# Kernel tuning notes

Measured on AMD Instinct MI355X. Metric: run time of the kernel, lower is better.

## Reference

```python
import jax, jax.numpy as jnp
import numpy as np

B, S, D = 4, 4096, 256


def setup_inputs() -> dict:
    key = jax.random.key(0)
    k1, k2, k3 = jax.random.split(key, 3)
    x = jax.random.normal(k1, (B, S, D), dtype=jnp.float32)
    w_int = jax.random.randint(k2, (D, D), 0, 127, dtype=jnp.int32)  # quantized weight (out, in)
    scale = jax.random.uniform(k3, (D,), dtype=jnp.float32)          # per-output-channel scale
    return {"x": x, "w_int": w_int, "scale": scale}


def reference(x, w_int, scale):
    # self-attention: q = k = v = x, single head over feature dim D
    inv_sqrt_d = 1.0 / jnp.sqrt(jnp.asarray(D, dtype=x.dtype))
    scores = jnp.einsum('bqd,bkd->bqk', x, x) * inv_sqrt_d   # [B,S,S]
    probs = jax.nn.softmax(scores, axis=-1)
    attn = jnp.einsum('bqk,bkd->bqd', probs, x)              # [B,S,D]
    # quantized linear: dequantize then matmul (y = attn @ W^T)
    W = w_int.astype(x.dtype) * scale[:, None]               # [D_out, D_in]
    return jnp.einsum('bsd,od->bso', attn, W)
```

## Files before the change

### kernel.cpp

```cpp
#include <hip/hip_runtime.h>

typedef __bf16 bf16x8 __attribute__((ext_vector_type(8)));
typedef float f32x16 __attribute__((ext_vector_type(16)));
typedef unsigned short u16x8 __attribute__((ext_vector_type(8)));

constexpr int B = 4, S = 4096, D = 256;
constexpr float CSC = 0.09016844005556021f;

static __device__ __forceinline__ unsigned short f2bf(float f) {
  unsigned int u = __builtin_bit_cast(unsigned int, f);
  u = (u + 0x7fffu + ((u >> 16) & 1u)) >> 16;
  return (unsigned short)u;
}

static __device__ __forceinline__ float bf2f(unsigned short u) {
  unsigned int v = ((unsigned int)u) << 16;
  return __builtin_bit_cast(float, v);
}

static __device__ __forceinline__ unsigned int pk2bf(float lo, float hi) {
  unsigned int r;
  asm("v_cvt_pk_bf16_f32 %0, %1, %2" : "=v"(r) : "v"(lo), "v"(hi));
  return r;
}

static __device__ __forceinline__ void gld16(const void* g, void* l) {
  __builtin_amdgcn_global_load_lds(
      (const __attribute__((address_space(1))) unsigned int*)g,
      (__attribute__((address_space(3))) unsigned int*)l, 16, 0, 0);
}

#define FENCE_V4()                                                \
  do {                                                            \
    asm volatile("s_waitcnt vmcnt(4) lgkmcnt(0)" ::: "memory");   \
    __builtin_amdgcn_s_barrier();                                 \
    asm volatile("" ::: "memory");                                \
  } while (0)
#define FENCE_V8()                                                \
  do {                                                            \
    asm volatile("s_waitcnt vmcnt(8) lgkmcnt(0)" ::: "memory");   \
    __builtin_amdgcn_s_barrier();                                 \
    asm volatile("" ::: "memory");                                \
  } while (0)
#define FENCE_LG()                                                \
  do {                                                            \
    asm volatile("s_waitcnt lgkmcnt(0)" ::: "memory");            \
    __builtin_amdgcn_s_barrier();                                 \
    asm volatile("" ::: "memory");                                \
  } while (0)
#define FENCE_ALL0()                                              \
  do {                                                            \
    asm volatile("s_waitcnt vmcnt(0) lgkmcnt(0)" ::: "memory");   \
    __builtin_amdgcn_s_barrier();                                 \
    asm volatile("" ::: "memory");                                \
  } while (0)

__global__ __launch_bounds__(256) void k_prep(const float* __restrict__ x,
                                              unsigned short* __restrict__ xK,
                                              unsigned short* __restrict__ xV) {
  __shared__ unsigned short T[64][72];
  __shared__ unsigned short R[64][72];
  int bid = blockIdx.x;
  int b = bid >> 8, rem = bid & 255;
  int s0 = (rem >> 2) * 64, d0 = (rem & 3) * 64;
  int j = threadIdx.x & 63, i0 = threadIdx.x >> 6;
#pragma unroll
  for (int k = 0; k < 16; ++k) {
    int i = k * 4 + i0;
    int idx = (b * S + s0 + i) * D + d0 + j;
    unsigned short v = f2bf(x[idx]);
    T[j][i] = v;
    R[i][j] = v;
  }
  __syncthreads();
  int t = s0 >> 6;
#pragma unroll
  for (int p = 0; p < 2; ++p) {
    int cc = p * 256 + threadIdx.x;
    int sl8 = cc >> 6, row = cc & 63;
    u16x8 v = *(const u16x8*)&R[row][sl8 * 8];
    int dg = d0 + sl8 * 8;
    int s = dg >> 4, hi = (dg >> 3) & 1;
    size_t off = ((((size_t)(b * 64 + t) * 16 + s) * 2 + hi) * 64 + row) * 8;
    *(u16x8*)(xK + off) = v;
  }
#pragma unroll
  for (int p = 0; p < 2; ++p) {
    int cc = p * 256 + threadIdx.x;
    int c = cc >> 7, hi = (cc >> 6) & 1, dl = cc & 63;
    u16x8 v = *(const u16x8*)&T[dl][c * 16 + hi * 8];
    size_t off = ((((size_t)(b * 64 + t) * 4 + c) * 2 + hi) * 256 + (d0 + dl)) * 8;
    *(u16x8*)(xV + off) = v;
  }
}

__global__ __launch_bounds__(256) void k_deqw(const int* __restrict__ w,
                                              unsigned short* __restrict__ wK) {
  int o = blockIdx.x, d = threadIdx.x;
  unsigned short v = f2bf((float)w[o * 256 + d]);
  wK[(((d >> 4) * 2 + ((d >> 3) & 1)) * 256 + o) * 8 + (d & 7)] = v;
}

__global__ __launch_bounds__(512, 2) void k_attn(const unsigned short* __restrict__ xK,
                                                 const unsigned short* __restrict__ xV,
                                                 unsigned short* __restrict__ PO0,
                                                 unsigned short* __restrict__ PO1,
                                                 float* __restrict__ ML) {
  __shared__ __align__(16) char smem[132096];

  int tid = threadIdx.x;
  int w = tid >> 6, lane = tid & 63;
  int q5 = lane & 31, hi = lane >> 5;
  int pair = w >> 1, dh = w & 1;

  int bid = blockIdx.x;
  int swz = (bid & 7) * 32 + (bid >> 3);
  int h = swz & 1;
  int qg = swz >> 1;
  int q0 = qg * 128;
  int bat = q0 >> 12;
  int qloc = q0 & (S - 1);

  int qrow = qloc + pair * 32 + q5;
  const unsigned short* Qb =
      xK + (size_t)(bat * 64 + (qrow >> 6)) * 16384 + hi * 512 + (qrow & 63) * 8;
  bf16x8 qf[16];
#pragma unroll
  for (int s = 0; s < 16; ++s) qf[s] = *(const bf16x8*)(Qb + s * 1024);

  f32x16 acc[8];
#pragma unroll
  for (int dt = 0; dt < 8; ++dt)
#pragma unroll
    for (int j = 0; j < 16; ++j) acc[dt][j] = 0.f;
  float l_lane = 0.f;
  unsigned int paw[8];

  const char* xKb = (const char*)xK + (size_t)(bat * 64 + h * 32) * 32768;
  const char* xVb = (const char*)xV + (size_t)(bat * 64 + h * 32) * 32768;

  auto STAGE_K = [&](int itile, int bb) {
    char* Kd = smem + bb * 32768;
    const char* srcK = xKb + (size_t)itile * 32768;
#pragma unroll
    for (int i = 0; i < 4; ++i) {
      int off = (w * 2 + (i >> 1)) * 2048 + (i & 1) * 1024;
      gld16(srcK + off + lane * 16, Kd + off);
    }
  };
  auto STAGE_V = [&](int itile, int bb) {
    char* Vd = smem + 65536 + bb * 32768;
    const char* srcV = xVb + (size_t)itile * 32768;
#pragma unroll
    for (int i = 0; i < 4; ++i) {
      int off = (w >> 1) * 8192 + ((w & 1) * 4 + i) * 1024;
      gld16(srcV + off + lane * 16, Vd + off);
    }
  };

  auto QK = [&](int bb, f32x16& st) {
    const char* Kt = smem + bb * 32768 + hi * 1024 + dh * 512 + q5 * 16;
#pragma unroll
    for (int j = 0; j < 16; ++j) st[j] = 0.f;
    __builtin_amdgcn_s_setprio(1);
#pragma unroll
    for (int s = 0; s < 16; ++s) {
      bf16x8 kf = *(const bf16x8*)(Kt + s * 2048);
      st = __builtin_amdgcn_mfma_f32_32x32x16_bf16(kf, qf[s], st, 0, 0, 0);
    }
    __builtin_amdgcn_s_setprio(0);
  };
  auto PV = [&](int bb) {
    union PA { unsigned int u[4]; bf16x8 v; };
    PA pa0, pa1;
    pa0.u[0] = paw[0]; pa0.u[1] = paw[1]; pa0.u[2] = paw[2]; pa0.u[3] = paw[3];
    pa1.u[0] = paw[4]; pa1.u[1] = paw[5]; pa1.u[2] = paw[6]; pa1.u[3] = paw[7];
    __builtin_amdgcn_s_setprio(1);
#pragma unroll
    for (int s2i = 0; s2i < 2; ++s2i) {
      const char* Vt = smem + 65536 + bb * 32768 + (dh * 2 + s2i) * 8192 +
                       hi * 4096 + q5 * 16;
      bf16x8 pa = (s2i == 0) ? pa0.v : pa1.v;
#pragma unroll
      for (int dt = 0; dt < 8; ++dt) {
        bf16x8 vf = *(const bf16x8*)(Vt + dt * 512);
        acc[dt] = __builtin_amdgcn_mfma_f32_32x32x16_bf16(vf, pa, acc[dt], 0, 0, 0);
      }
    }
    __builtin_amdgcn_s_setprio(0);
  };
  auto SM = [&](const f32x16& st) {
    unsigned int pk[8];
    float ps = 0.f;
#pragma unroll
    for (int a = 0; a < 8; ++a) {
      float lo = exp2f(st[2 * a] * CSC);
      float hh = exp2f(st[2 * a + 1] * CSC);
      ps += lo + hh;
      pk[a] = pk2bf(lo, hh);
    }
    l_lane += ps;
    unsigned int a0 = pk[0], b0 = pk[2];
    unsigned int a1 = pk[1], b1 = pk[3];
    unsigned int a2 = pk[4], b2 = pk[6];
    unsigned int a3 = pk[5], b3 = pk[7];
    asm volatile("v_permlane32_swap_b32 %0, %1" : "+v"(a0), "+v"(b0));
    asm volatile("v_permlane32_swap_b32 %0, %1" : "+v"(a1), "+v"(b1));
    asm volatile("v_permlane32_swap_b32 %0, %1" : "+v"(a2), "+v"(b2));
    asm volatile("v_permlane32_swap_b32 %0, %1" : "+v"(a3), "+v"(b3));
    paw[0] = a0; paw[1] = a1; paw[2] = b0; paw[3] = b1;
    paw[4] = a2; paw[5] = a3; paw[6] = b2; paw[7] = b3;
  };

  STAGE_K(0, 0);
  STAGE_V(0, 0);
  STAGE_K(1, 1);
  FENCE_V8();
  {
    f32x16 st;
    QK(0, st);
    SM(st);
  }
  STAGE_V(1, 1);

  for (int t = 1; t < 32; ++t) {
    int cur = t & 1;
    FENCE_V4();
    if (t < 31) STAGE_K(t + 1, cur ^ 1);
    f32x16 st;
    QK(cur, st);
    PV(cur ^ 1);
    SM(st);
    FENCE_LG();
    if (t < 31) STAGE_V(t + 1, cur ^ 1);
  }

  FENCE_ALL0();
  PV(1);

  float lw = l_lane + __shfl_xor(l_lane, 32, 64);
  float* LX = (float*)(smem + 131072);
  if (lane < 32) LX[w * 32 + q5] = lw;
  __syncthreads();
  float l_tot = lw + LX[(w ^ 1) * 32 + q5];
  if (dh == 0 && lane < 32) {
    int row = q0 + pair * 32 + q5;
    ML[((size_t)h * 16384 + row) * 2 + 0] = 0.f;
    ML[((size_t)h * 16384 + row) * 2 + 1] = l_tot;
  }
  __syncthreads();

  unsigned short* Pb2 = (h == 0) ? PO0 : PO1;
#pragma unroll
  for (int rh = 0; rh < 2; ++rh) {
    float* slot = (float*)(smem + w * 16384);
#pragma unroll
    for (int dt4 = 0; dt4 < 4; ++dt4) {
#pragma unroll
      for (int r = 0; r < 16; ++r) {
        int dloc = dt4 * 32 + (r & 3) + 8 * (r >> 2) + 4 * hi;
        slot[dloc * 32 + q5] = acc[rh * 4 + dt4][r];
      }
    }
    __syncthreads();
    if (dh == rh) {
      const float* pslot = (const float*)(smem + (w ^ 1) * 16384);
#pragma unroll
      for (int dt4 = 0; dt4 < 4; ++dt4) {
#pragma unroll
        for (int r = 0; r < 16; ++r) {
          int dloc = dt4 * 32 + (r & 3) + 8 * (r >> 2) + 4 * hi;
          acc[rh * 4 + dt4][r] += pslot[dloc * 32 + q5];
        }
      }
      char* E = smem + w * 16384;
#pragma unroll
      for (int dt4 = 0; dt4 < 4; ++dt4) {
#pragma unroll
        for (int a = 0; a < 4; ++a) {
          int dl = dt4 * 32 + 8 * a + 4 * hi;
          *(unsigned int*)(E + q5 * 272 + dl * 2) =
              pk2bf(acc[rh * 4 + dt4][4 * a + 0], acc[rh * 4 + dt4][4 * a + 1]);
          *(unsigned int*)(E + q5 * 272 + dl * 2 + 4) =
              pk2bf(acc[rh * 4 + dt4][4 * a + 2], acc[rh * 4 + dt4][4 * a + 3]);
        }
      }
      asm volatile("s_waitcnt lgkmcnt(0)" ::: "memory");
#pragma unroll
      for (int i = 0; i < 8; ++i) {
        int qr = i * 4 + (lane >> 4);
        int ch = lane & 15;
        u16x8 v = *(const u16x8*)(E + qr * 272 + ch * 16);
        *(u16x8*)(Pb2 + (size_t)(q0 + pair * 32 + qr) * 256 + rh * 128 + ch * 8) = v;
      }
    }
    __syncthreads();
  }
}

__global__ __launch_bounds__(512, 2) void k_gemm(const unsigned short* __restrict__ PO0,
                                                 const unsigned short* __restrict__ PO1,
                                                 const float* __restrict__ ML,
                                                 const unsigned short* __restrict__ wK,
                                                 const float* __restrict__ scale,
                                                 float* __restrict__ out) {
  __shared__ __align__(16) char Wl[131072];
  int tid = threadIdx.x;
  int w = tid >> 6, lane = tid & 63;
  int q5 = lane & 31, hi = lane >> 5;
  int msub = w & 1, oq = w >> 1;
  int m0 = blockIdx.x * 64;

#pragma unroll
  for (int i = 0; i < 16; ++i) {
    int off = (i * 512 + tid) * 16;
    gld16((const char*)wK + off, Wl + off);
  }

  int row = m0 + msub * 32 + q5;
  float il = 1.f / (ML[(size_t)row * 2 + 1] + ML[((size_t)16384 + row) * 2 + 1]);

  bf16x8 af[16];
#pragma unroll
  for (int s = 0; s < 16; ++s) {
    u16x8 a0 = *(const u16x8*)(PO0 + (size_t)row * 256 + s * 16 + hi * 8);
    u16x8 a1 = *(const u16x8*)(PO1 + (size_t)row * 256 + s * 16 + hi * 8);
    union { unsigned int u[4]; bf16x8 v; } cv;
#pragma unroll
    for (int e = 0; e < 4; ++e) {
      float lo = (bf2f(a0[2 * e]) + bf2f(a1[2 * e])) * il;
      float hh = (bf2f(a0[2 * e + 1]) + bf2f(a1[2 * e + 1])) * il;
      cv.u[e] = pk2bf(lo, hh);
    }
    af[s] = cv.v;
  }

  asm volatile("s_waitcnt vmcnt(0)" ::: "memory");
  __builtin_amdgcn_s_barrier();

  f32x16 acc[2];
#pragma unroll
  for (int t = 0; t < 2; ++t)
#pragma unroll
    for (int j = 0; j < 16; ++j) acc[t][j] = 0.f;

#pragma unroll
  for (int t = 0; t < 2; ++t) {
    int obase = (oq * 2 + t) * 32;
    const char* Wt = Wl + hi * 4096 + (obase + q5) * 16;
#pragma unroll
    for (int s = 0; s < 16; ++s) {
      bf16x8 wf = *(const bf16x8*)(Wt + s * 8192);
      acc[t] = __builtin_amdgcn_mfma_f32_32x32x16_bf16(af[s], wf, acc[t], 0, 0, 0);
    }
  }

#pragma unroll
  for (int t = 0; t < 2; ++t) {
    int o = (oq * 2 + t) * 32 + q5;
    float sc = scale[o];
#pragma unroll
    for (int r = 0; r < 16; ++r) {
      int mr = m0 + msub * 32 + (r & 3) + 8 * (r >> 2) + 4 * hi;
      out[(size_t)mr * 256 + o] = acc[t][r] * sc;
    }
  }
}

extern "C" void kernel_launch(void* const* d_in, const int* in_sizes, int n_in,
                              void* d_out, int out_size, void* d_ws, size_t ws_size,
                              hipStream_t stream) {
  (void)in_sizes; (void)n_in; (void)out_size; (void)ws_size;
  const float* x = (const float*)d_in[0];
  const int* w_int = (const int*)d_in[1];
  const float* scale = (const float*)d_in[2];
  float* out = (float*)d_out;

  char* ws = (char*)d_ws;
  unsigned short* xK  = (unsigned short*)(ws);
  unsigned short* xV  = (unsigned short*)(ws + 8388608);
  unsigned short* wK  = (unsigned short*)(ws + 16777216);
  float*          ML  = (float*)(ws + 16908288);
  unsigned short* PO0 = (unsigned short*)(ws + 17170432);
  unsigned short* PO1 = (unsigned short*)(ws + 25559040);

  k_prep<<<dim3(1024), dim3(256), 0, stream>>>(x, xK, xV);
  k_deqw<<<dim3(256), dim3(256), 0, stream>>>(w_int, wK);
  k_attn<<<dim3(256), dim3(512), 0, stream>>>(xK, xV, PO0, PO1, ML);
  k_gemm<<<dim3(256), dim3(512), 0, stream>>>(PO0, PO1, ML, wK, scale, out);
}
```

Before: 101.3 us.

## Triple-buffer V tiles to drop the mid-iteration barrier in attention loop

The V shared-memory staging moves from double to triple buffering, which grows LDS to 160 KB. K and V for the next tile are now issued together at the top of each iteration. This removes the second lgkmcnt wait plus workgroup barrier that previously sat between PV/softmax and staging the next V tile. The cost is extra LDS, which rules out co-residency of a second block. The vmcnt-based fence logic still covers correctness because the pending loads are always the just-issued tile.

```diff
diff --git a/kernel.cpp b/kernel.cpp
--- a/kernel.cpp
+++ b/kernel.cpp
@@ -42,12 +42,6 @@
     __builtin_amdgcn_s_barrier();                                 \
     asm volatile("" ::: "memory");                                \
   } while (0)
-#define FENCE_LG()                                                \
-  do {                                                            \
-    asm volatile("s_waitcnt lgkmcnt(0)" ::: "memory");            \
-    __builtin_amdgcn_s_barrier();                                 \
-    asm volatile("" ::: "memory");                                \
-  } while (0)
 #define FENCE_ALL0()                                              \
   do {                                                            \
     asm volatile("s_waitcnt vmcnt(0) lgkmcnt(0)" ::: "memory");   \
@@ -106,7 +100,7 @@
                                                  unsigned short* __restrict__ PO0,
                                                  unsigned short* __restrict__ PO1,
                                                  float* __restrict__ ML) {
-  __shared__ __align__(16) char smem[132096];
+  __shared__ __align__(16) char smem[163840];
 
   int tid = threadIdx.x;
   int w = tid >> 6, lane = tid & 63;
@@ -139,8 +133,8 @@
   const char* xKb = (const char*)xK + (size_t)(bat * 64 + h * 32) * 32768;
   const char* xVb = (const char*)xV + (size_t)(bat * 64 + h * 32) * 32768;
 
-  auto STAGE_K = [&](int itile, int bb) {
-    char* Kd = smem + bb * 32768;
+  auto STAGE_K = [&](int itile, int kb) {
+    char* Kd = smem + kb * 32768;
     const char* srcK = xKb + (size_t)itile * 32768;
 #pragma unroll
     for (int i = 0; i < 4; ++i) {
@@ -148,8 +142,8 @@
       gld16(srcK + off + lane * 16, Kd + off);
     }
   };
-  auto STAGE_V = [&](int itile, int bb) {
-    char* Vd = smem + 65536 + bb * 32768;
+  auto STAGE_V = [&](int itile, int vb) {
+    char* Vd = smem + 65536 + vb * 32768;
     const char* srcV = xVb + (size_t)itile * 32768;
 #pragma unroll
     for (int i = 0; i < 4; ++i) {
@@ -158,8 +152,8 @@
     }
   };
 
-  auto QK = [&](int bb, f32x16& st) {
-    const char* Kt = smem + bb * 32768 + hi * 1024 + dh * 512 + q5 * 16;
+  auto QK = [&](int kb, f32x16& st) {
+    const char* Kt = smem + kb * 32768 + hi * 1024 + dh * 512 + q5 * 16;
 #pragma unroll
     for (int j = 0; j < 16; ++j) st[j] = 0.f;
     __builtin_amdgcn_s_setprio(1);
@@ -170,7 +164,7 @@
     }
     __builtin_amdgcn_s_setprio(0);
   };
-  auto PV = [&](int bb) {
+  auto PV = [&](int vb) {
     union PA { unsigned int u[4]; bf16x8 v; };
     PA pa0, pa1;
     pa0.u[0] = paw[0]; pa0.u[1] = paw[1]; pa0.u[2] = paw[2]; pa0.u[3] = paw[3];
@@ -178,7 +172,7 @@
     __builtin_amdgcn_s_setprio(1);
 #pragma unroll
     for (int s2i = 0; s2i < 2; ++s2i) {
-      const char* Vt = smem + 65536 + bb * 32768 + (dh * 2 + s2i) * 8192 +
+      const char* Vt = smem + 65536 + vb * 32768 + (dh * 2 + s2i) * 8192 +
                        hi * 4096 + q5 * 16;
       bf16x8 pa = (s2i == 0) ? pa0.v : pa1.v;
 #pragma unroll
@@ -215,24 +209,24 @@
   STAGE_K(0, 0);
   STAGE_V(0, 0);
   STAGE_K(1, 1);
+  STAGE_V(1, 1);
   FENCE_V8();
   {
     f32x16 st;
     QK(0, st);
     SM(st);
   }
-  STAGE_V(1, 1);
 
   for (int t = 1; t < 32; ++t) {
-    int cur = t & 1;
     FENCE_V4();
-    if (t < 31) STAGE_K(t + 1, cur ^ 1);
+    if (t < 31) {
+      STAGE_K(t + 1, (t + 1) & 1);
+      STAGE_V(t + 1, (t + 1) % 3);
+    }
     f32x16 st;
-    QK(cur, st);
-    PV(cur ^ 1);
+    QK(t & 1, st);
+    PV((t - 1) % 3);
     SM(st);
-    FENCE_LG();
-    if (t < 31) STAGE_V(t + 1, cur ^ 1);
   }
 
   FENCE_ALL0();
```

Result: no change. 101.3 us (+0.0%).
